# Kernel optimization log

Measured on AMD Instinct MI355X. Metric: run time of the kernel, lower is better.

Reference implementation:

```python
import jax, jax.numpy as jnp
import numpy as np
from itertools import combinations_with_replacement

INPUT_DIM = 128
DEGREE = 2

# Static index arrays for degree-2 terms (i<=j), matching
# combinations_with_replacement order.
_pairs = np.array(list(combinations_with_replacement(range(INPUT_DIM), DEGREE)), dtype=np.int32)
I_IDX = jnp.asarray(_pairs[:, 0])  # [d*(d+1)/2]
J_IDX = jnp.asarray(_pairs[:, 1])


def setup_inputs() -> dict:
    key = jax.random.key(0)
    k1, k2, k3 = jax.random.split(key, 3)
    B, D, N = 8192, INPUT_DIM, 512
    num_outputs = D + D * (D + 1) // 2  # 8384
    x = jax.random.normal(k1, (B, D), dtype=jnp.float32)
    weights = jax.random.normal(k2, (N, num_outputs), dtype=jnp.float32)
    bias = jax.random.normal(k3, (N,), dtype=jnp.float32)
    return {"x": x, "weights": weights, "bias": bias}


def reference(x, weights, bias):
    # Polynomial feature expansion: [x, x_i * x_j for i<=j]
    poly = x[:, I_IDX] * x[:, J_IDX]          # [B, d*(d+1)/2]
    feats = jnp.concatenate([x, poly], axis=1)  # [B, num_outputs]
    # (output.unsqueeze(1) * weights.unsqueeze(0)).sum(-1) == feats @ weights.T
    return jnp.einsum('bo,no->bn', feats, weights) + bias
```

## Files before the change

kernel.cpp:

```cpp
#include <hip/hip_runtime.h>
#include <hip/hip_bf16.h>
#include <stdint.h>

#define D_IN   128
#define NPOLY  8256
#define KDIM   8384
#define B_ROWS 8192
#define N_COLS 512

#define TBL_OFF   0
#define TBL_BYTES (NPOLY * 2)
#define WBF_OFF   (TBL_OFF + TBL_BYTES)
#define WBF_BYTES ((size_t)N_COLS * KDIM * 2)
#define FEA_OFF   (WBF_OFF + WBF_BYTES)
#define FEA_BYTES ((size_t)B_ROWS * KDIM * 2)
#define WS_NEED   (FEA_OFF + FEA_BYTES)

typedef __attribute__((ext_vector_type(8))) short    bf16x8_t;
typedef __attribute__((ext_vector_type(8))) float    f32x8_t;
typedef __attribute__((ext_vector_type(4))) float    f32x4_t;

__device__ __forceinline__ uint16_t f2bf(float f) {
  union { float f; uint32_t u; } c; c.f = f;
  uint32_t u = c.u;
  uint32_t r = (u + 0x7fffu + ((u >> 16) & 1u)) >> 16;
  return (uint16_t)r;
}

__device__ __forceinline__ void async_load16(void* lds_dst, const void* g_src) {
  __builtin_amdgcn_global_load_lds(
      (const __attribute__((address_space(1))) void*)g_src,
      (__attribute__((address_space(3))) void*)lds_dst,
      16, 0, 0);
}

__global__ void build_table(uint16_t* __restrict__ tbl) {
  int p = blockIdx.x * 256 + threadIdx.x;
  if (p >= NPOLY) return;
  float t = 66049.0f - 8.0f * (float)p;
  int i = (int)((257.0f - sqrtf(t)) * 0.5f);
  if (i < 0) i = 0; if (i > 127) i = 127;
  while (i < 127 && ((i + 1) * (257 - (i + 1))) / 2 <= p) ++i;
  while (i > 0 && (i * (257 - i)) / 2 > p) --i;
  int j = i + (p - (i * (257 - i)) / 2);
  tbl[p] = (uint16_t)((i << 8) | j);
}

__global__ void wconv(const float* __restrict__ w, uint16_t* __restrict__ wb) {
  int g = blockIdx.x * 256 + threadIdx.x;
  if (g >= (N_COLS * KDIM) / 8) return;
  f32x8_t v = *(const f32x8_t*)(w + (size_t)g * 8);
  bf16x8_t o;
#pragma unroll
  for (int e = 0; e < 8; ++e) o[e] = (short)f2bf(v[e]);
  *(bf16x8_t*)(wb + (size_t)g * 8) = o;
}

__global__ __launch_bounds__(256) void feat_gen(
    const float* __restrict__ x, const uint16_t* __restrict__ tbl,
    uint16_t* __restrict__ feats) {
  __shared__ float xs[D_IN];
  __shared__ __align__(16) uint16_t pr[KDIM];
  const int b = blockIdx.x;
  const int tid = threadIdx.x;
  if (tid < D_IN) {
    float v = x[(size_t)b * D_IN + tid];
    xs[tid] = v;
    pr[tid] = f2bf(v);
  }
  __syncthreads();
#pragma unroll 4
  for (int p = tid; p < NPOLY; p += 256) {
    uint32_t t = tbl[p];
    pr[D_IN + p] = f2bf(xs[t >> 8] * xs[t & 255u]);
  }
  __syncthreads();
  const bf16x8_t* src = (const bf16x8_t*)pr;
  bf16x8_t* dst = (bf16x8_t*)(feats + (size_t)b * KDIM);
  for (int g = tid; g < KDIM / 8; g += 256) dst[g] = src[g];
}

__global__ void init_out(float* __restrict__ out, const float* __restrict__ bias) {
  int idx = blockIdx.x * 256 + threadIdx.x;
  f32x4_t bv = *(const f32x4_t*)(bias + ((idx * 4) & (N_COLS - 1)));
  *(f32x4_t*)(out + (size_t)idx * 4) = bv;
}

#define BMT 128
#define BNT 128
#define BKT 64
#define KSTEPS 131
#define KCUT 66

__global__ __launch_bounds__(256, 2) void gemm_poly(
    const uint16_t* __restrict__ A,
    const uint16_t* __restrict__ W,
    float* __restrict__ out) {
  __shared__ __align__(16) uint16_t sA[2][BMT * BKT];
  __shared__ __align__(16) uint16_t sW[2][BNT * BKT];

  const int tid  = threadIdx.x;
  const int lane = tid & 63;
  const int wv   = tid >> 6;
  const int wr   = wv >> 1;
  const int wc   = wv & 1;
  const int hi   = lane >> 4;
  const int lr   = lane & 15;

  const int b0 = blockIdx.x * BMT;
  const int n0 = blockIdx.y * BNT;
  const int kt0 = (blockIdx.z == 0) ? 0 : KCUT;
  const int kt1 = (blockIdx.z == 0) ? KCUT : KSTEPS;

  int rowq[4], cbxq[4];
#pragma unroll
  for (int q = 0; q < 4; ++q) {
    int L = q * 4096 + tid * 16;
    int row = L >> 7;
    int cb  = L & 127;
    rowq[q] = row;
    cbxq[q] = cb ^ ((row & 7) << 4);
  }

  int offA[4][2], offW[4][2];
#pragma unroll
  for (int f = 0; f < 4; ++f) {
    int rowA = wr * 64 + f * 16 + lr;
    int rowW = wc * 64 + f * 16 + lr;
#pragma unroll
    for (int kh = 0; kh < 2; ++kh) {
      int kb = kh * 64 + hi * 16;
      offA[f][kh] = rowA * 128 + (kb ^ ((rowA & 7) << 4));
      offW[f][kh] = rowW * 128 + (kb ^ ((rowW & 7) << 4));
    }
  }

  f32x4_t acc[4][4];
#pragma unroll
  for (int mf = 0; mf < 4; ++mf)
#pragma unroll
    for (int nf = 0; nf < 4; ++nf) {
      f32x4_t z = {0.f, 0.f, 0.f, 0.f};
      acc[mf][nf] = z;
    }

  const char* Ab = (const char*)A;
  const char* Wb = (const char*)W;

#define STAGE(buf, kt)                                                         \
  {                                                                            \
    _Pragma("unroll")                                                          \
    for (int q = 0; q < 4; ++q) {                                              \
      const char* srcA =                                                       \
          Ab + ((size_t)(b0 + rowq[q]) * KDIM + (kt) * BKT) * 2 + cbxq[q];     \
      async_load16((char*)sA[buf] + q * 4096 + tid * 16, srcA);                \
    }                                                                          \
    _Pragma("unroll")                                                          \
    for (int q = 0; q < 4; ++q) {                                              \
      const char* srcW =                                                       \
          Wb + ((size_t)(n0 + rowq[q]) * KDIM + (kt) * BKT) * 2 + cbxq[q];     \
      async_load16((char*)sW[buf] + q * 4096 + tid * 16, srcW);                \
    }                                                                          \
  }

  STAGE(0, kt0);
  __syncthreads();
  int cur = 0;
  for (int kt = kt0; kt < kt1; ++kt) {
    if (kt + 1 < kt1) STAGE(cur ^ 1, kt + 1);
    bf16x8_t a[4][2], b[4][2];
#pragma unroll
    for (int mf = 0; mf < 4; ++mf)
#pragma unroll
      for (int kh = 0; kh < 2; ++kh)
        a[mf][kh] = *(const bf16x8_t*)((const char*)sA[cur] + offA[mf][kh]);
#pragma unroll
    for (int nf = 0; nf < 4; ++nf)
#pragma unroll
      for (int kh = 0; kh < 2; ++kh)
        b[nf][kh] = *(const bf16x8_t*)((const char*)sW[cur] + offW[nf][kh]);
    __builtin_amdgcn_s_setprio(1);
#pragma unroll
    for (int mf = 0; mf < 4; ++mf)
#pragma unroll
      for (int nf = 0; nf < 4; ++nf) {
        acc[mf][nf] = __builtin_amdgcn_mfma_f32_16x16x32_bf16(
            a[mf][0], b[nf][0], acc[mf][nf], 0, 0, 0);
        acc[mf][nf] = __builtin_amdgcn_mfma_f32_16x16x32_bf16(
            a[mf][1], b[nf][1], acc[mf][nf], 0, 0, 0);
      }
    __builtin_amdgcn_s_setprio(0);
    __syncthreads();
    cur ^= 1;
  }

#pragma unroll
  for (int mf = 0; mf < 4; ++mf) {
    int row = b0 + wr * 64 + mf * 16 + hi * 4;
#pragma unroll
    for (int nf = 0; nf < 4; ++nf) {
      int col = n0 + wc * 64 + nf * 16 + lr;
#pragma unroll
      for (int r = 0; r < 4; ++r) {
        atomicAdd(&out[(size_t)(row + r) * N_COLS + col], acc[mf][nf][r]);
      }
    }
  }
#undef STAGE
}

__global__ void naive_poly(const float* __restrict__ x, const float* __restrict__ w,
                           const float* __restrict__ bias, float* __restrict__ out) {
  size_t o = (size_t)blockIdx.x * 256 + threadIdx.x;
  if (o >= (size_t)B_ROWS * N_COLS) return;
  int n = (int)(o >> 13);
  int b = (int)(o & (B_ROWS - 1));
  const float* xr = x + (size_t)b * D_IN;
  const float* wr = w + (size_t)n * KDIM;
  float acc = bias[n];
  for (int k = 0; k < D_IN; ++k) acc += wr[k] * xr[k];
  int p = D_IN;
  for (int i = 0; i < D_IN; ++i) {
    float xi = xr[i];
    for (int j = i; j < D_IN; ++j) acc += wr[p++] * xi * xr[j];
  }
  out[(size_t)b * N_COLS + n] = acc;
}

extern "C" void kernel_launch(void* const* d_in, const int* in_sizes, int n_in,
                              void* d_out, int out_size, void* d_ws, size_t ws_size,
                              hipStream_t stream) {
  const float* x    = (const float*)d_in[0];
  const float* w    = (const float*)d_in[1];
  const float* bias = (const float*)d_in[2];
  float* out = (float*)d_out;

  if (ws_size < WS_NEED) {
    naive_poly<<<(B_ROWS * N_COLS) / 256, 256, 0, stream>>>(x, w, bias, out);
    return;
  }

  char* ws = (char*)d_ws;
  uint16_t* tbl = (uint16_t*)(ws + TBL_OFF);
  uint16_t* wb  = (uint16_t*)(ws + WBF_OFF);
  uint16_t* fe  = (uint16_t*)(ws + FEA_OFF);

  build_table<<<(NPOLY + 255) / 256, 256, 0, stream>>>(tbl);
  wconv<<<(N_COLS * KDIM / 8 + 255) / 256, 256, 0, stream>>>(w, wb);
  feat_gen<<<B_ROWS, 256, 0, stream>>>(x, tbl, fe);
  init_out<<<(B_ROWS * N_COLS / 4) / 256, 256, 0, stream>>>(out, bias);
  gemm_poly<<<dim3(B_ROWS / BMT, N_COLS / BNT, 2), 256, 0, stream>>>(fe, wb, out);
}
```

Baseline: 201.4 us.

## Load weight fragments directly from global, single-buffer A, 3-way split-K with XCD swizzle

Merges the table, weight-conversion and bias-init kernels into one prep launch. The GEMM stops staging W through LDS and has each lane read its bf16 weight fragments straight from global memory, which relies on cache hits. A is kept in one LDS buffer instead of two. Split-K goes from 2 to 3 chunks, launch bounds allow 3 blocks per CU, and a block-index swizzle groups tiles per XCD. Dropping double buffering exposes A load latency behind the barriers, and the direct global W reads may stall the MFMA pipeline.

New measurement: 277.6 us. +37.8%, slower.

```diff
diff --git a/kernel.cpp b/kernel.cpp
--- a/kernel.cpp
+++ b/kernel.cpp
@@ -34,26 +34,36 @@
       16, 0, 0);
 }
 
-__global__ void build_table(uint16_t* __restrict__ tbl) {
-  int p = blockIdx.x * 256 + threadIdx.x;
-  if (p >= NPOLY) return;
-  float t = 66049.0f - 8.0f * (float)p;
-  int i = (int)((257.0f - sqrtf(t)) * 0.5f);
-  if (i < 0) i = 0; if (i > 127) i = 127;
-  while (i < 127 && ((i + 1) * (257 - (i + 1))) / 2 <= p) ++i;
-  while (i > 0 && (i * (257 - i)) / 2 > p) --i;
-  int j = i + (p - (i * (257 - i)) / 2);
-  tbl[p] = (uint16_t)((i << 8) | j);
-}
-
-__global__ void wconv(const float* __restrict__ w, uint16_t* __restrict__ wb) {
-  int g = blockIdx.x * 256 + threadIdx.x;
-  if (g >= (N_COLS * KDIM) / 8) return;
-  f32x8_t v = *(const f32x8_t*)(w + (size_t)g * 8);
-  bf16x8_t o;
-#pragma unroll
-  for (int e = 0; e < 8; ++e) o[e] = (short)f2bf(v[e]);
-  *(bf16x8_t*)(wb + (size_t)g * 8) = o;
+#define NB_INIT 4096
+#define NB_WCNV 2096
+#define NB_TBL  33
+__global__ void prep(const float* __restrict__ w, const float* __restrict__ bias,
+                     float* __restrict__ out, uint16_t* __restrict__ wb,
+                     uint16_t* __restrict__ tbl) {
+  int blk = blockIdx.x;
+  int tid = threadIdx.x;
+  if (blk < NB_INIT) {
+    int idx = blk * 256 + tid;
+    f32x4_t bv = *(const f32x4_t*)(bias + ((idx * 4) & (N_COLS - 1)));
+    *(f32x4_t*)(out + (size_t)idx * 4) = bv;
+  } else if (blk < NB_INIT + NB_WCNV) {
+    int g = (blk - NB_INIT) * 256 + tid;
+    f32x8_t v = *(const f32x8_t*)(w + (size_t)g * 8);
+    bf16x8_t o;
+#pragma unroll
+    for (int e = 0; e < 8; ++e) o[e] = (short)f2bf(v[e]);
+    *(bf16x8_t*)(wb + (size_t)g * 8) = o;
+  } else {
+    int p = (blk - NB_INIT - NB_WCNV) * 256 + tid;
+    if (p >= NPOLY) return;
+    float t = 66049.0f - 8.0f * (float)p;
+    int i = (int)((257.0f - sqrtf(t)) * 0.5f);
+    if (i < 0) i = 0; if (i > 127) i = 127;
+    while (i < 127 && ((i + 1) * (257 - (i + 1))) / 2 <= p) ++i;
+    while (i > 0 && (i * (257 - i)) / 2 > p) --i;
+    int j = i + (p - (i * (257 - i)) / 2);
+    tbl[p] = (uint16_t)((i << 8) | j);
+  }
 }
 
 __global__ __launch_bounds__(256) void feat_gen(
@@ -80,24 +90,17 @@
   for (int g = tid; g < KDIM / 8; g += 256) dst[g] = src[g];
 }
 
-__global__ void init_out(float* __restrict__ out, const float* __restrict__ bias) {
-  int idx = blockIdx.x * 256 + threadIdx.x;
-  f32x4_t bv = *(const f32x4_t*)(bias + ((idx * 4) & (N_COLS - 1)));
-  *(f32x4_t*)(out + (size_t)idx * 4) = bv;
-}
-
 #define BMT 128
 #define BNT 128
 #define BKT 64
 #define KSTEPS 131
-#define KCUT 66
-
-__global__ __launch_bounds__(256, 2) void gemm_poly(
+#define KP     44
+
+__global__ __launch_bounds__(256, 3) void gemm_poly(
     const uint16_t* __restrict__ A,
     const uint16_t* __restrict__ W,
     float* __restrict__ out) {
-  __shared__ __align__(16) uint16_t sA[2][BMT * BKT];
-  __shared__ __align__(16) uint16_t sW[2][BNT * BKT];
+  __shared__ __align__(16) uint16_t sA[BMT * BKT];
 
   const int tid  = threadIdx.x;
   const int lane = tid & 63;
@@ -107,10 +110,17 @@
   const int hi   = lane >> 4;
   const int lr   = lane & 15;
 
-  const int b0 = blockIdx.x * BMT;
-  const int n0 = blockIdx.y * BNT;
-  const int kt0 = (blockIdx.z == 0) ? 0 : KCUT;
-  const int kt1 = (blockIdx.z == 0) ? KCUT : KSTEPS;
+  int bid = blockIdx.x;
+  int lin = (bid & 7) * 96 + (bid >> 3);
+  int bx  = lin / 12;
+  int rem = lin - bx * 12;
+  int by  = rem / 3;
+  int bz  = rem - by * 3;
+
+  const int b0  = bx * BMT;
+  const int n0  = by * BNT;
+  const int kt0 = bz * KP;
+  const int kt1 = (bz == 2) ? KSTEPS : kt0 + KP;
 
   int rowq[4], cbxq[4];
 #pragma unroll
@@ -122,17 +132,22 @@
     cbxq[q] = cb ^ ((row & 7) << 4);
   }
 
-  int offA[4][2], offW[4][2];
+  int offA[4][2];
 #pragma unroll
   for (int f = 0; f < 4; ++f) {
     int rowA = wr * 64 + f * 16 + lr;
-    int rowW = wc * 64 + f * 16 + lr;
 #pragma unroll
     for (int kh = 0; kh < 2; ++kh) {
       int kb = kh * 64 + hi * 16;
       offA[f][kh] = rowA * 128 + (kb ^ ((rowA & 7) << 4));
-      offW[f][kh] = rowW * 128 + (kb ^ ((rowW & 7) << 4));
-    }
+    }
+  }
+
+  uint32_t wOff[4];
+#pragma unroll
+  for (int nf = 0; nf < 4; ++nf) {
+    int rowW = n0 + wc * 64 + nf * 16 + lr;
+    wOff[nf] = (uint32_t)rowW * (KDIM * 2) + (uint32_t)hi * 16;
   }
 
   f32x4_t acc[4][4];
@@ -147,38 +162,32 @@
   const char* Ab = (const char*)A;
   const char* Wb = (const char*)W;
 
-#define STAGE(buf, kt)                                                         \
+#define STAGE(kt)                                                              \
   {                                                                            \
     _Pragma("unroll")                                                          \
     for (int q = 0; q < 4; ++q) {                                              \
       const char* srcA =                                                       \
           Ab + ((size_t)(b0 + rowq[q]) * KDIM + (kt) * BKT) * 2 + cbxq[q];     \
-      async_load16((char*)sA[buf] + q * 4096 + tid * 16, srcA);                \
+      async_load16((char*)sA + q * 4096 + tid * 16, srcA);                     \
     }                                                                          \
-    _Pragma("unroll")                                                          \
-    for (int q = 0; q < 4; ++q) {                                              \
-      const char* srcW =                                                       \
-          Wb + ((size_t)(n0 + rowq[q]) * KDIM + (kt) * BKT) * 2 + cbxq[q];     \
-      async_load16((char*)sW[buf] + q * 4096 + tid * 16, srcW);                \
-    }                                                                          \
-  }
-
-  STAGE(0, kt0);
-  __syncthreads();
-  int cur = 0;
+  }
+
+  STAGE(kt0);
   for (int kt = kt0; kt < kt1; ++kt) {
-    if (kt + 1 < kt1) STAGE(cur ^ 1, kt + 1);
-    bf16x8_t a[4][2], b[4][2];
+    __syncthreads();
+    const char* wk = Wb + (uint32_t)kt * 128;
+    bf16x8_t b[4][2];
+#pragma unroll
+    for (int nf = 0; nf < 4; ++nf) {
+      b[nf][0] = *(const bf16x8_t*)(wk + wOff[nf]);
+      b[nf][1] = *(const bf16x8_t*)(wk + wOff[nf] + 64);
+    }
+    bf16x8_t a[4][2];
 #pragma unroll
     for (int mf = 0; mf < 4; ++mf)
 #pragma unroll
       for (int kh = 0; kh < 2; ++kh)
-        a[mf][kh] = *(const bf16x8_t*)((const char*)sA[cur] + offA[mf][kh]);
-#pragma unroll
-    for (int nf = 0; nf < 4; ++nf)
-#pragma unroll
-      for (int kh = 0; kh < 2; ++kh)
-        b[nf][kh] = *(const bf16x8_t*)((const char*)sW[cur] + offW[nf][kh]);
+        a[mf][kh] = *(const bf16x8_t*)((const char*)sA + offA[mf][kh]);
     __builtin_amdgcn_s_setprio(1);
 #pragma unroll
     for (int mf = 0; mf < 4; ++mf)
@@ -191,7 +200,7 @@
       }
     __builtin_amdgcn_s_setprio(0);
     __syncthreads();
-    cur ^= 1;
+    if (kt + 1 < kt1) STAGE(kt + 1);
   }
 
 #pragma unroll
@@ -245,9 +254,7 @@
   uint16_t* wb  = (uint16_t*)(ws + WBF_OFF);
   uint16_t* fe  = (uint16_t*)(ws + FEA_OFF);
 
-  build_table<<<(NPOLY + 255) / 256, 256, 0, stream>>>(tbl);
-  wconv<<<(N_COLS * KDIM / 8 + 255) / 256, 256, 0, stream>>>(w, wb);
+  prep<<<NB_INIT + NB_WCNV + NB_TBL, 256, 0, stream>>>(w, bias, out, wb, tbl);
   feat_gen<<<B_ROWS, 256, 0, stream>>>(x, tbl, fe);
-  init_out<<<(B_ROWS * N_COLS / 4) / 256, 256, 0, stream>>>(out, bias);
-  gemm_poly<<<dim3(B_ROWS / BMT, N_COLS / BNT, 2), 256, 0, stream>>>(fe, wb, out);
-}
+  gemm_poly<<<768, 256, 0, stream>>>(fe, wb, out);
+}
```
